# Optimization experiments

Hardware: AMD Instinct MI355X
Metric: run time of the kernel (lower is better)

The kernel has to match this reference:

```python
import jax, jax.numpy as jnp
import numpy as np

B, N, M, D = 8, 2048, 2048, 512

def setup_inputs() -> dict:
    key = jax.random.key(0)
    ks = jax.random.split(key, 10)
    s = 1.0 / np.sqrt(D)  # torch Linear default init scale (approx)
    return {
        "lidar_features": jax.random.normal(ks[0], (B, N, D), jnp.float32),
        "camera_features": jax.random.normal(ks[1], (B, M, D), jnp.float32),
        "lidar_confidence": jax.random.uniform(ks[2], (B, N, 1), jnp.float32),
        "camera_confidence": jax.random.uniform(ks[3], (B, M, 1), jnp.float32),
        "Wq": jax.random.normal(ks[4], (D, D), jnp.float32) * s,
        "bq": jnp.zeros((D,), jnp.float32),
        "Wk": jax.random.normal(ks[5], (D, D), jnp.float32) * s,
        "bk": jnp.zeros((D,), jnp.float32),
        "Wv": jax.random.normal(ks[6], (D, D), jnp.float32) * s,
        "bv": jnp.zeros((D,), jnp.float32),
    }

def reference(lidar_features, camera_features, lidar_confidence, camera_confidence,
              Wq, bq, Wk, bk, Wv, bv):
    # torch nn.Linear: x @ W.T + b
    q = (jnp.einsum('bnd,ed->bne', lidar_features, Wq) + bq) * lidar_confidence
    k = jnp.einsum('bmd,ed->bme', camera_features, Wk) + bk
    v = jnp.einsum('bmd,ed->bme', camera_features, Wv) + bv
    # note: no 1/sqrt(d) scaling in the original; camera_confidence is unused
    scores = jnp.einsum('bne,bme->bnm', q, k)  # [B,N,M]
    attn = jax.nn.softmax(scores, axis=-1)
    fused = jnp.einsum('bnm,bme->bne', attn, v)
    return fused
```

## Files before the change

### kernel.cpp

```cpp
#include <hip/hip_runtime.h>
#include <hip/hip_bf16.h>

#define BB 8
#define NN 2048
#define MM 2048
#define DD 512

typedef __attribute__((ext_vector_type(8))) _Float16 f16x8;
typedef __attribute__((ext_vector_type(4))) float f32x4;
typedef __attribute__((ext_vector_type(8))) unsigned short u16x8;

__device__ __forceinline__ unsigned short f2h(float x){
  union { _Float16 h; unsigned short u; } cv;
  cv.h = (_Float16)x;
  return cv.u;
}
__device__ __forceinline__ float h2f(unsigned short u){
  union { unsigned short u; _Float16 h; } cv;
  cv.u = u;
  return (float)cv.h;
}
__device__ __forceinline__ f32x4 mfmah(f16x8 a, f16x8 b, f32x4 c){
  return __builtin_amdgcn_mfma_f32_16x16x32_f16(a, b, c, 0, 0, 0);
}

#define GLD16(gp, lp) __builtin_amdgcn_global_load_lds( \
    (const __attribute__((address_space(1))) void*)(gp), \
    (__attribute__((address_space(3))) void*)(lp), 16, 0, 0)

#define WAITVM(n) __builtin_amdgcn_s_waitcnt(0xF70 | (n))

__device__ __forceinline__ void swz_xyz(int& bn, int& bm, int& bz){
  int f = ((int)blockIdx.z * (int)gridDim.y + (int)blockIdx.y) * (int)gridDim.x
        + (int)blockIdx.x;
  bz = f & 7;
  int r = f >> 3;
  bn = r % (int)gridDim.x;
  bm = r / (int)gridDim.x;
}

__global__ __launch_bounds__(256) void cvt16_kernel(const float* __restrict__ in,
    unsigned short* __restrict__ out, int n4){
  int i = blockIdx.x*256 + threadIdx.x;
  const int stride = gridDim.x*256;
  for (; i < n4; i += stride){
    float4 v = ((const float4*)in)[i];
    ushort4 h; h.x=f2h(v.x); h.y=f2h(v.y); h.z=f2h(v.z); h.w=f2h(v.w);
    ((ushort4*)out)[i] = h;
  }
}

__global__ __launch_bounds__(256) void cam_prep(const float* __restrict__ cam,
    const float* __restrict__ c2,
    unsigned short* __restrict__ camH,
    float* __restrict__ svec){
  const int t = threadIdx.x;
  const int l = t & 63;
  const size_t row = (size_t)blockIdx.x*4 + (t >> 6);
  const float4* r4 = (const float4*)(cam + row*DD);
  const float4* c4 = (const float4*)c2;
  float4 v0 = r4[l*2],   v1 = r4[l*2+1];
  float4 a0 = c4[l*2],   a1 = c4[l*2+1];
  float p = v0.x*a0.x + v0.y*a0.y + v0.z*a0.z + v0.w*a0.w
          + v1.x*a1.x + v1.y*a1.y + v1.z*a1.z + v1.w*a1.w;
  for (int o = 32; o; o >>= 1) p += __shfl_xor(p, o);
  if (l == 0) svec[row] = p;
  ushort4 h0; h0.x=f2h(v0.x); h0.y=f2h(v0.y); h0.z=f2h(v0.z); h0.w=f2h(v0.w);
  ushort4 h1; h1.x=f2h(v1.x); h1.y=f2h(v1.y); h1.z=f2h(v1.z); h1.w=f2h(v1.w);
  ushort4* dst = (ushort4*)(camH + row*DD);
  dst[l*2]   = h0;
  dst[l*2+1] = h1;
}

__global__ __launch_bounds__(256) void at_kernel(const float* __restrict__ Wq,
                                                 const float* __restrict__ Wk,
                                                 unsigned short* __restrict__ atH){
  const int i0 = blockIdx.x * 32, j0 = blockIdx.y * 32;
  __shared__ float q_s[32][33];
  __shared__ float k_s[32][33];
  const int t = threadIdx.x;
  const int tx = t & 15, ty = t >> 4;
  float acc[2][2] = {{0.f,0.f},{0.f,0.f}};
  for (int e0 = 0; e0 < DD; e0 += 32){
    __syncthreads();
#pragma unroll
    for (int p = 0; p < 4; ++p){
      int idx = t + 256*p;
      int e = idx >> 5, c = idx & 31;
      q_s[e][c] = Wq[(size_t)(e0+e)*DD + i0 + c];
      k_s[e][c] = Wk[(size_t)(e0+e)*DD + j0 + c];
    }
    __syncthreads();
#pragma unroll 8
    for (int e = 0; e < 32; ++e){
      float q0 = q_s[e][2*tx], q1 = q_s[e][2*tx+1];
      float k0 = k_s[e][2*ty], k1 = k_s[e][2*ty+1];
      acc[0][0] += k0*q0; acc[0][1] += k0*q1;
      acc[1][0] += k1*q0; acc[1][1] += k1*q1;
    }
  }
#pragma unroll
  for (int a = 0; a < 2; ++a)
#pragma unroll
    for (int b = 0; b < 2; ++b)
      atH[(size_t)(j0 + 2*ty + a)*DD + i0 + 2*tx + b] = f2h(acc[a][b]);
}

__global__ __launch_bounds__(256) void c2_kernel(const float* __restrict__ bq,
                                                 const float* __restrict__ Wk,
                                                 float* __restrict__ c2){
  int d = blockIdx.x * 256 + threadIdx.x;
  float a = 0.f;
  for (int e = 0; e < DD; ++e) a += bq[e] * Wk[(size_t)e*DD + d];
  c2[d] = a;
}

template<int MODE>
__global__ __launch_bounds__(256) void gemm_h128(
    const unsigned short* __restrict__ Ag, long sA, int lda,
    const unsigned short* __restrict__ Bg, long sB, int ldb,
    unsigned short* __restrict__ O, long sO, int ldo,
    const float* __restrict__ bias)
{
  __shared__ __attribute__((aligned(16))) unsigned short Ah[128][40];
  __shared__ __attribute__((aligned(16))) unsigned short Bh[128][40];

  int bn, bm, bz; swz_xyz(bn, bm, bz);
  const int t = threadIdx.x;
  const int lane = t & 63, w = t >> 6;
  const int wrow = w >> 1, wcol = w & 1;
  const int lr = lane & 15, lk = (lane >> 4) << 3;

  f32x4 acc[4][4];
#pragma unroll
  for (int m = 0; m < 4; ++m)
#pragma unroll
    for (int n = 0; n < 4; ++n){ f32x4 z = {0.f,0.f,0.f,0.f}; acc[m][n] = z; }

  const unsigned short* Ap = Ag + (size_t)bz*(size_t)sA + ((size_t)bm*128)*(size_t)lda;
  const unsigned short* Bp = Bg + (size_t)bz*(size_t)sB + ((size_t)bn*128)*(size_t)ldb;

  const int sr = t >> 2;
  const int sc = (t & 3) * 8;

  for (int k0 = 0; k0 < DD; k0 += 32){
    __syncthreads();
#pragma unroll
    for (int p = 0; p < 2; ++p){
      int r = sr + 64*p;
      *(u16x8*)&Ah[r][sc] = *(const u16x8*)(Ap + (size_t)r*lda + k0 + sc);
      *(u16x8*)&Bh[r][sc] = *(const u16x8*)(Bp + (size_t)r*ldb + k0 + sc);
    }
    __syncthreads();

    f16x8 af[4], bf[4];
#pragma unroll
    for (int m = 0; m < 4; ++m) af[m] = *(const f16x8*)&Ah[wrow*64 + m*16 + lr][lk];
#pragma unroll
    for (int n = 0; n < 4; ++n) bf[n] = *(const f16x8*)&Bh[wcol*64 + n*16 + lr][lk];
#pragma unroll
    for (int m = 0; m < 4; ++m)
#pragma unroll
      for (int n = 0; n < 4; ++n)
        acc[m][n] = mfmah(af[m], bf[n], acc[m][n]);
  }

  const int orow = bm*128 + wrow*64;
  const int ocol = bn*128 + wcol*64;
#pragma unroll
  for (int m = 0; m < 4; ++m){
#pragma unroll
    for (int n = 0; n < 4; ++n){
      int col  = ocol + n*16 + lr;
      int row0 = orow + m*16 + ((lane >> 4) << 2);
#pragma unroll
      for (int r = 0; r < 4; ++r){
        int row = row0 + r;
        float v = acc[m][n][r];
        if constexpr (MODE == 1) v += bias[row];
        O[(size_t)bz*(size_t)sO + (size_t)row*ldo + col] = f2h(v);
      }
    }
  }
}

__global__ __launch_bounds__(512) void gemm_scores(
    const unsigned short* __restrict__ Th, const unsigned short* __restrict__ camH,
    unsigned short* __restrict__ O,
    const float* __restrict__ conf, const float* __restrict__ svec)
{
  __shared__ __attribute__((aligned(16))) unsigned short Ah[128][40];
  __shared__ __attribute__((aligned(16))) unsigned short Bh[256][40];

  int bn, bm, bz; swz_xyz(bn, bm, bz);
  const int t = threadIdx.x;
  const int lane = t & 63, w = t >> 6;
  const int wrow = w >> 2, wcol = w & 3;
  const int lr = lane & 15, lk = (lane >> 4) << 3;

  f32x4 acc[4][4];
#pragma unroll
  for (int m = 0; m < 4; ++m)
#pragma unroll
    for (int n = 0; n < 4; ++n){ f32x4 z = {0.f,0.f,0.f,0.f}; acc[m][n] = z; }

  const unsigned short* Ap = Th   + (size_t)bz*((size_t)NN*DD) + ((size_t)bm*128)*DD;
  const unsigned short* Bp = camH + (size_t)bz*((size_t)MM*DD) + ((size_t)bn*256)*DD;

  const int sr = t >> 2;
  const int sc = (t & 3) * 8;

  for (int k0 = 0; k0 < DD; k0 += 32){
    __syncthreads();
    *(u16x8*)&Ah[sr][sc] = *(const u16x8*)(Ap + (size_t)sr*DD + k0 + sc);
#pragma unroll
    for (int p = 0; p < 2; ++p){
      int r = sr + 128*p;
      *(u16x8*)&Bh[r][sc] = *(const u16x8*)(Bp + (size_t)r*DD + k0 + sc);
    }
    __syncthreads();

    f16x8 af[4], bf[4];
#pragma unroll
    for (int m = 0; m < 4; ++m) af[m] = *(const f16x8*)&Ah[wrow*64 + m*16 + lr][lk];
#pragma unroll
    for (int n = 0; n < 4; ++n) bf[n] = *(const f16x8*)&Bh[wcol*64 + n*16 + lr][lk];
#pragma unroll
    for (int m = 0; m < 4; ++m)
#pragma unroll
      for (int n = 0; n < 4; ++n)
        acc[m][n] = mfmah(af[m], bf[n], acc[m][n]);
  }

  const int orow0 = bm*128 + wrow*64;
  const int ocol0 = bn*256 + wcol*64;
  const size_t obase = (size_t)bz*((size_t)NN*MM);
#pragma unroll
  for (int m = 0; m < 4; ++m){
#pragma unroll
    for (int n = 0; n < 4; ++n){
      int col  = ocol0 + n*16 + lr;
      float sv = svec[bz*MM + col];
      int row0 = orow0 + m*16 + ((lane >> 4) << 2);
#pragma unroll
      for (int r = 0; r < 4; ++r){
        int row = row0 + r;
        O[obase + (size_t)row*MM + col]
            = f2h(conf[bz*NN + row] * (acc[m][n][r] + sv));
      }
    }
  }
}

__global__ __launch_bounds__(256) void softmax_h(unsigned short* __restrict__ scores){
  const size_t row = blockIdx.x;
  unsigned short* pr = scores + row * (size_t)MM;
  const int t = threadIdx.x;

  u16x8 v = ((const u16x8*)pr)[t];
  float x[8];
#pragma unroll
  for (int j = 0; j < 8; ++j) x[j] = h2f(v[j]);

  float mx = x[0];
#pragma unroll
  for (int j = 1; j < 8; ++j) mx = fmaxf(mx, x[j]);
  for (int o = 32; o; o >>= 1) mx = fmaxf(mx, __shfl_xor(mx, o));
  __shared__ float red[4];
  if ((t & 63) == 0) red[t >> 6] = mx;
  __syncthreads();
  mx = fmaxf(fmaxf(red[0], red[1]), fmaxf(red[2], red[3]));

  float e[8], s = 0.f;
#pragma unroll
  for (int j = 0; j < 8; ++j){ e[j] = __expf(x[j] - mx); s += e[j]; }
  for (int o = 32; o; o >>= 1) s += __shfl_xor(s, o);
  __syncthreads();
  if ((t & 63) == 0) red[t >> 6] = s;
  __syncthreads();
  float inv = 1.f / (red[0] + red[1] + red[2] + red[3]);

  u16x8 pv;
#pragma unroll
  for (int j = 0; j < 8; ++j) pv[j] = f2h(e[j] * inv);
  ((u16x8*)pr)[t] = pv;
}

__global__ __launch_bounds__(512) void gemm_pv(
    const unsigned short* __restrict__ P,
    const unsigned short* __restrict__ V,
    float* __restrict__ O)
{
  __shared__ unsigned short Ah[2][64][64];
  __shared__ unsigned short Bh[2][256][64];

  int bn, bm, bz; swz_xyz(bn, bm, bz);
  const int t = threadIdx.x;
  const int lane = t & 63, w = t >> 6;
  const int lr = lane & 15, lc0 = lane >> 4;

  const unsigned short* Ap = P + (size_t)bz*((size_t)NN*MM) + ((size_t)bm*64)*MM;
  const unsigned short* Bp = V + (size_t)bz*((size_t)DD*MM) + ((size_t)bn*256)*MM;

  const int arow = 8*w + (lane >> 3);
  const int alc  = (lane & 7) ^ (arow & 7);
  const unsigned short* gA = Ap + (size_t)arow*MM + alc*8;
  const int brow = 32*w + (lane >> 3);
  const int blc  = (lane & 7) ^ (brow & 7);
  const unsigned short* gB = Bp + (size_t)brow*MM + blc*8;

#define PV_STAGE(bufi, kofs) do {                                   \
    GLD16(gA + (kofs),                 &Ah[bufi][8*w][0]);          \
    GLD16(gB + (kofs),                 &Bh[bufi][32*w     ][0]);    \
    GLD16(gB + (kofs) + (size_t)8*MM,  &Bh[bufi][32*w +  8][0]);    \
    GLD16(gB + (kofs) + (size_t)16*MM, &Bh[bufi][32*w + 16][0]);    \
    GLD16(gB + (kofs) + (size_t)24*MM, &Bh[bufi][32*w + 24][0]);    \
  } while(0)

  f32x4 acc[4][2];
#pragma unroll
  for (int m = 0; m < 4; ++m)
#pragma unroll
    for (int n = 0; n < 2; ++n){ f32x4 z = {0.f,0.f,0.f,0.f}; acc[m][n] = z; }

  PV_STAGE(0, 0);
  WAITVM(0);
  __builtin_amdgcn_s_barrier();
  __builtin_amdgcn_sched_barrier(0);

  for (int tt = 0; tt < 32; ++tt){
    const int buf = tt & 1;
    if (tt < 31) PV_STAGE(buf^1, (size_t)(tt+1)*64);
    f16x8 af[4][2], bf[2][2];
#pragma unroll
    for (int m = 0; m < 4; ++m){
      int row = m*16 + lr;
#pragma unroll
      for (int ks = 0; ks < 2; ++ks){
        int pc = (ks*4 + lc0) ^ (row & 7);
        af[m][ks] = *(const f16x8*)&Ah[buf][row][pc*8];
      }
    }
#pragma unroll
    for (int n = 0; n < 2; ++n){
      int row = w*32 + n*16 + lr;
#pragma unroll
      for (int ks = 0; ks < 2; ++ks){
        int pc = (ks*4 + lc0) ^ (row & 7);
        bf[n][ks] = *(const f16x8*)&Bh[buf][row][pc*8];
      }
    }
    __builtin_amdgcn_s_setprio(1);
#pragma unroll
    for (int m = 0; m < 4; ++m)
#pragma unroll
      for (int n = 0; n < 2; ++n){
        acc[m][n] = mfmah(af[m][0], bf[n][0], acc[m][n]);
        acc[m][n] = mfmah(af[m][1], bf[n][1], acc[m][n]);
      }
    __builtin_amdgcn_s_setprio(0);

    WAITVM(0);
    __builtin_amdgcn_s_barrier();
    __builtin_amdgcn_sched_barrier(0);
  }
#undef PV_STAGE

  const int orow0 = bm*64;
  const int ocol0 = bn*256 + w*32;
#pragma unroll
  for (int m = 0; m < 4; ++m){
#pragma unroll
    for (int n = 0; n < 2; ++n){
      int col  = ocol0 + n*16 + lr;
      int row0 = orow0 + m*16 + ((lane >> 4) << 2);
#pragma unroll
      for (int r = 0; r < 4; ++r){
        int row = row0 + r;
        O[(size_t)bz*((size_t)NN*DD) + (size_t)row*DD + col] = acc[m][n][r];
      }
    }
  }
}

extern "C" void kernel_launch(void* const* d_in, const int* in_sizes, int n_in,
                              void* d_out, int out_size, void* d_ws, size_t ws_size,
                              hipStream_t stream) {
  const float* lidar  = (const float*)d_in[0];
  const float* camera = (const float*)d_in[1];
  const float* lconf  = (const float*)d_in[2];
  const float* Wq = (const float*)d_in[4];
  const float* bq = (const float*)d_in[5];
  const float* Wk = (const float*)d_in[6];
  const float* Wv = (const float*)d_in[8];
  const float* bv = (const float*)d_in[9];
  float* out = (float*)d_out;

  char* ws = (char*)d_ws;
  unsigned short* scores = (unsigned short*)(ws + 0);
  unsigned short* liH    = (unsigned short*)(ws + 0);
  unsigned short* atH    = (unsigned short*)(ws + 16777216);
  unsigned short* wvH    = (unsigned short*)(ws + 17301504);
  float*          c2     = (float*)(ws + 17825792);
  unsigned short* Th     = (unsigned short*)(ws + 134217728);
  unsigned short* camH   = (unsigned short*)(ws + 150994944);
  unsigned short* Vt     = (unsigned short*)(ws + 167772160);
  float*          svec   = (float*)(ws + 184549376);

  c2_kernel<<<dim3(2), 256, 0, stream>>>(bq, Wk, c2);
  cam_prep<<<dim3(BB*MM/4), 256, 0, stream>>>(camera, c2, camH, svec);
  cvt16_kernel<<<dim3(2048), 256, 0, stream>>>(lidar,  liH,  BB*NN*DD/4);
  cvt16_kernel<<<dim3(256),  256, 0, stream>>>(Wv,     wvH,  DD*DD/4);
  at_kernel<<<dim3(16,16), 256, 0, stream>>>(Wq, Wk, atH);

  gemm_h128<0><<<dim3(DD/128, NN/128, BB), 256, 0, stream>>>(
      liH, (long)NN*DD, DD,  atH, 0, DD,
      Th, (long)NN*DD, DD, nullptr);

  gemm_h128<1><<<dim3(MM/128, DD/128, BB), 256, 0, stream>>>(
      wvH, 0, DD,  camH, (long)MM*DD, DD,
      Vt, (long)DD*MM, MM, bv);

  gemm_scores<<<dim3(MM/256, NN/128, BB), 512, 0, stream>>>(
      Th, camH, scores, lconf, svec);

  softmax_h<<<dim3(BB*NN), 256, 0, stream>>>(scores);

  gemm_pv<<<dim3(DD/256, NN/64, BB), 512, 0, stream>>>(
      scores, Vt, out);
}
```

Measured before the change: 202.4 us.

## Double-buffer scores GEMM with direct global-to-LDS loads and XOR swizzle

The scores GEMM now uses double-buffered LDS tiles, filled by direct global-to-LDS loads (the GLD16 macro) that prefetch the next K step while MFMAs run on the current one. Padding is replaced by an XOR swizzle of 16-byte chunks to avoid LDS bank conflicts, and wave priority is raised around the MFMA block. The aim is to hide global load latency and drop one barrier per iteration. In exchange it doubles LDS use, which may lower occupancy, and it depends on the GLD16 and WAITVM macros defined elsewhere in the file.

```diff
diff --git a/kernel.cpp b/kernel.cpp
--- a/kernel.cpp
+++ b/kernel.cpp
@@ -189,48 +189,72 @@
     unsigned short* __restrict__ O,
     const float* __restrict__ conf, const float* __restrict__ svec)
 {
-  __shared__ __attribute__((aligned(16))) unsigned short Ah[128][40];
-  __shared__ __attribute__((aligned(16))) unsigned short Bh[256][40];
+  __shared__ unsigned short Ah[2][128][32];
+  __shared__ unsigned short Bh[2][256][32];
 
   int bn, bm, bz; swz_xyz(bn, bm, bz);
   const int t = threadIdx.x;
   const int lane = t & 63, w = t >> 6;
   const int wrow = w >> 2, wcol = w & 3;
-  const int lr = lane & 15, lk = (lane >> 4) << 3;
-
-  f32x4 acc[4][4];
-#pragma unroll
-  for (int m = 0; m < 4; ++m)
-#pragma unroll
-    for (int n = 0; n < 4; ++n){ f32x4 z = {0.f,0.f,0.f,0.f}; acc[m][n] = z; }
+  const int lr = lane & 15;
+  const int c4 = lane >> 4;
 
   const unsigned short* Ap = Th   + (size_t)bz*((size_t)NN*DD) + ((size_t)bm*128)*DD;
   const unsigned short* Bp = camH + (size_t)bz*((size_t)MM*DD) + ((size_t)bn*256)*DD;
 
-  const int sr = t >> 2;
-  const int sc = (t & 3) * 8;
-
-  for (int k0 = 0; k0 < DD; k0 += 32){
-    __syncthreads();
-    *(u16x8*)&Ah[sr][sc] = *(const u16x8*)(Ap + (size_t)sr*DD + k0 + sc);
-#pragma unroll
-    for (int p = 0; p < 2; ++p){
-      int r = sr + 128*p;
-      *(u16x8*)&Bh[r][sc] = *(const u16x8*)(Bp + (size_t)r*DD + k0 + sc);
-    }
-    __syncthreads();
-
+  const int sar  = w*16 + (lane >> 2);
+  const int salc = (lane & 3) ^ (sar & 3);
+  const unsigned short* gA = Ap + (size_t)sar*DD + salc*8;
+  const int sbr  = w*32 + (lane >> 2);
+  const int sblc = (lane & 3) ^ (sbr & 3);
+  const unsigned short* gB = Bp + (size_t)sbr*DD + sblc*8;
+
+#define SC_STAGE(bufi, kofs) do {                                  \
+    GLD16(gA + (kofs),                 &Ah[bufi][w*16     ][0]);   \
+    GLD16(gB + (kofs),                 &Bh[bufi][w*32     ][0]);   \
+    GLD16(gB + (kofs) + (size_t)16*DD, &Bh[bufi][w*32 + 16][0]);   \
+  } while(0)
+
+  f32x4 acc[4][4];
+#pragma unroll
+  for (int m = 0; m < 4; ++m)
+#pragma unroll
+    for (int n = 0; n < 4; ++n){ f32x4 z = {0.f,0.f,0.f,0.f}; acc[m][n] = z; }
+
+  SC_STAGE(0, 0);
+  WAITVM(0);
+  __builtin_amdgcn_s_barrier();
+  __builtin_amdgcn_sched_barrier(0);
+
+  for (int tt = 0; tt < 16; ++tt){
+    const int buf = tt & 1;
+    if (tt < 15) SC_STAGE(buf^1, (size_t)(tt+1)*32);
     f16x8 af[4], bf[4];
 #pragma unroll
-    for (int m = 0; m < 4; ++m) af[m] = *(const f16x8*)&Ah[wrow*64 + m*16 + lr][lk];
-#pragma unroll
-    for (int n = 0; n < 4; ++n) bf[n] = *(const f16x8*)&Bh[wcol*64 + n*16 + lr][lk];
+    for (int m = 0; m < 4; ++m){
+      int row = wrow*64 + m*16 + lr;
+      int pc  = c4 ^ (row & 3);
+      af[m] = *(const f16x8*)&Ah[buf][row][pc*8];
+    }
+#pragma unroll
+    for (int n = 0; n < 4; ++n){
+      int row = wcol*64 + n*16 + lr;
+      int pc  = c4 ^ (row & 3);
+      bf[n] = *(const f16x8*)&Bh[buf][row][pc*8];
+    }
+    __builtin_amdgcn_s_setprio(1);
 #pragma unroll
     for (int m = 0; m < 4; ++m)
 #pragma unroll
       for (int n = 0; n < 4; ++n)
         acc[m][n] = mfmah(af[m], bf[n], acc[m][n]);
-  }
+    __builtin_amdgcn_s_setprio(0);
+
+    WAITVM(0);
+    __builtin_amdgcn_s_barrier();
+    __builtin_amdgcn_sched_barrier(0);
+  }
+#undef SC_STAGE
 
   const int orow0 = bm*128 + wrow*64;
   const int ocol0 = bn*256 + wcol*64;
```

After: 199.1 us. About the same (-1.7%).
